# Performance work log

Measured on AMD Instinct MI355X. Metric: run time of the kernel, lower is better.

Reference implementation:

```python
import jax, jax.numpy as jnp
import numpy as np

LOC_SIZE, LOC_EMB = 100000, 256
TIM_SIZE, TIM_EMB = 48, 64
UID_SIZE, UID_EMB = 5000, 128
HID = 512
B, T = 64, 128
L_HIST, G = 1024, 4  # 256 history groups of size 4


def setup_inputs() -> dict:
    key = jax.random.key(0)
    ks = jax.random.split(key, 16)
    s = 0.02
    inp = {
        "loc": jax.random.randint(ks[0], (B, T), 0, LOC_SIZE),
        "tim": jax.random.randint(ks[1], (B, T), 0, TIM_SIZE),
        "input_lengths": jax.random.randint(ks[2], (B,), 1, T + 1),
        "history_loc": jax.random.randint(ks[3], (B, L_HIST), 0, LOC_SIZE),
        "history_tim": jax.random.randint(ks[4], (B, L_HIST), 0, TIM_SIZE),
        "history_uid": jax.random.randint(ks[5], (B, L_HIST), 0, UID_SIZE),
        "group_size": G,
        "emb_loc": jax.random.normal(ks[6], (LOC_SIZE, LOC_EMB), jnp.float32) * s,
        "emb_tim": jax.random.normal(ks[7], (TIM_SIZE, TIM_EMB), jnp.float32) * s,
        "emb_uid": jax.random.normal(ks[8], (UID_SIZE, UID_EMB), jnp.float32) * s,
        "W_attn": jax.random.normal(ks[9], (HID, LOC_EMB + TIM_EMB + UID_EMB), jnp.float32) * s,
        "b_attn": jnp.zeros((HID,), jnp.float32),
        "W_ih": jax.random.normal(ks[10], (3 * HID, LOC_EMB + TIM_EMB), jnp.float32) * s,
        "b_ih": jnp.zeros((3 * HID,), jnp.float32),
        "W_hh": jax.random.normal(ks[11], (3 * HID, HID), jnp.float32) * s,
        "b_hh": jnp.zeros((3 * HID,), jnp.float32),
        "W_final": jax.random.normal(ks[12], (UID_SIZE, 3 * HID), jnp.float32) * s,
        "b_final": jnp.zeros((UID_SIZE,), jnp.float32),
    }
    return inp


def _gru(x_seq, W_ih, b_ih, W_hh, b_hh):
    # x_seq: [T, B, Din] -> outputs [T, B, H], PyTorch gate order (r, z, n)
    H = W_hh.shape[1]
    gx = jnp.einsum("tbd,gd->tbg", x_seq, W_ih) + b_ih  # [T,B,3H]
    h0 = jnp.zeros((x_seq.shape[1], H), x_seq.dtype)

    def step(h, gx_t):
        gh = h @ W_hh.T + b_hh
        xr, xz, xn = jnp.split(gx_t, 3, axis=-1)
        hr, hz, hn = jnp.split(gh, 3, axis=-1)
        r = jax.nn.sigmoid(xr + hr)
        z = jax.nn.sigmoid(xz + hz)
        n = jnp.tanh(xn + r * hn)
        h_new = (1.0 - z) * n + z * h
        return h_new, h_new

    _, outs = jax.lax.scan(step, h0, gx)
    return outs  # [T,B,H]


def reference(loc, tim, input_lengths, history_loc, history_tim, history_uid,
              group_size, emb_loc, emb_tim, emb_uid, W_attn, b_attn,
              W_ih, b_ih, W_hh, b_hh, W_final, b_final):
    Bn, Tn = loc.shape
    # current-trajectory embeddings -> GRU (dropout is identity in eval)
    x = jnp.concatenate([emb_loc[loc], emb_tim[tim]], axis=-1)  # [B,T,Din]
    outs = _gru(jnp.swapaxes(x, 0, 1), W_ih, b_ih, W_hh, b_hh)  # [T,B,H]
    outs = jnp.swapaxes(outs, 0, 1)                              # [B,T,H]
    last = outs[jnp.arange(Bn), input_lengths - 1]               # [B,H]

    # history pooling: groups of size G; uid emb averaged within group,
    # loc/tim embeddings taken at each group's first element
    Gc = group_size
    n_groups = history_uid.shape[1] // Gc
    uid_h = emb_uid[history_uid].reshape(Bn, n_groups, Gc, -1).mean(axis=2)  # [B,N,Du]
    loc_h = emb_loc[history_loc[:, ::Gc]]                                    # [B,N,Dl]
    tim_h = emb_tim[history_tim[:, ::Gc]]                                    # [B,N,Dt]
    hist = jnp.concatenate([loc_h, tim_h, uid_h], axis=-1)
    hist = jnp.tanh(jnp.einsum("bnd,hd->bnh", hist, W_attn) + b_attn)        # [B,N,H]

    # 'dot' attention: replaces the nested python-loop scoring
    energies = jnp.einsum("bh,bnh->bn", last, hist)
    attn_w = jax.nn.softmax(energies, axis=-1)
    context = jnp.einsum("bn,bnh->bh", attn_w, hist)

    out = jnp.concatenate([last, context, last], axis=-1)  # [B,3H]
    y = out @ W_final.T + b_final                          # [B,U]
    # original assigns y (one row) into score[t] of shape [T,U] -> broadcast over T
    score = jnp.broadcast_to(y[:, None, :], (Bn, Tn, y.shape[-1]))
    return score
```

## Files before the change

kernel.cpp:

```cpp
#include <hip/hip_runtime.h>
#include <hip/hip_bf16.h>


typedef __attribute__((ext_vector_type(8))) short bf16x8;
typedef __attribute__((ext_vector_type(4))) float f32x4;
typedef __attribute__((ext_vector_type(4))) unsigned short u16x4;
typedef __attribute__((ext_vector_type(2))) unsigned long long u64x2;
typedef unsigned long long u64;

__device__ inline unsigned short f2bf(float x) {
  __hip_bfloat16 b = __float2bfloat16(x);
  return __builtin_bit_cast(unsigned short, b);
}
__device__ inline bf16x8 pack8(float4 a, float4 b) {
  bf16x8 w;
  w[0]=(short)f2bf(a.x); w[1]=(short)f2bf(a.y); w[2]=(short)f2bf(a.z); w[3]=(short)f2bf(a.w);
  w[4]=(short)f2bf(b.x); w[5]=(short)f2bf(b.y); w[6]=(short)f2bf(b.z); w[7]=(short)f2bf(b.w);
  return w;
}

__global__ __launch_bounds__(256)
void gemm_gx_f(const int* __restrict__ loc, const int* __restrict__ tim,
               const float* __restrict__ eloc, const float* __restrict__ etim,
               const float* __restrict__ W_ih, const float* __restrict__ b_ih,
               float* __restrict__ gx) {
  constexpr int LDR = 40, K = 320, N = 1536;
  __shared__ short Asl[128 * LDR];
  __shared__ short Bsl[128 * LDR];
  const int tid = threadIdx.x;
  const int lane = tid & 63, wid = tid >> 6;
  const int wr = wid >> 1, wc = wid & 1;
  const int m16 = lane & 15, g4 = lane >> 4;
  const int bm = blockIdx.y * 128, bn = blockIdx.x * 128;
  const int srow = tid >> 1, shalf = tid & 1;
  const int grow = bm + srow;
  const int t_ = grow >> 6, b_ = grow & 63;
  const float* aloc = eloc + (size_t)loc[b_ * 128 + t_] * 256 + (shalf << 4);
  const float* atim = etim + (size_t)tim[b_ * 128 + t_] * 64 + (shalf << 4);
  const float* bbase = W_ih + (size_t)(bn + srow) * K + (shalf << 4);
  float4 a0, a1, a2, a3, w0, w1, w2, w3;
  {
    a0 = ((const float4*)aloc)[0]; a1 = ((const float4*)aloc)[1];
    a2 = ((const float4*)aloc)[2]; a3 = ((const float4*)aloc)[3];
    w0 = ((const float4*)bbase)[0]; w1 = ((const float4*)bbase)[1];
    w2 = ((const float4*)bbase)[2]; w3 = ((const float4*)bbase)[3];
  }
  f32x4 acc[4][4] = {};
  for (int k0 = 0; k0 < K; k0 += 32) {
    short* arow = Asl + srow * LDR + (shalf << 4);
    *(bf16x8*)(arow)     = pack8(a0, a1);
    *(bf16x8*)(arow + 8) = pack8(a2, a3);
    short* brow = Bsl + srow * LDR + (shalf << 4);
    *(bf16x8*)(brow)     = pack8(w0, w1);
    *(bf16x8*)(brow + 8) = pack8(w2, w3);
    __syncthreads();
    if (k0 + 32 < K) {
      const int kn = k0 + 32;
      const float* ap = (kn < 256) ? (aloc + kn) : (atim + (kn - 256));
      a0 = ((const float4*)ap)[0]; a1 = ((const float4*)ap)[1];
      a2 = ((const float4*)ap)[2]; a3 = ((const float4*)ap)[3];
      const float* bp = bbase + kn;
      w0 = ((const float4*)bp)[0]; w1 = ((const float4*)bp)[1];
      w2 = ((const float4*)bp)[2]; w3 = ((const float4*)bp)[3];
    }
    bf16x8 af[4], bfr[4];
#pragma unroll
    for (int i = 0; i < 4; ++i) {
      af[i]  = *(const bf16x8*)(Asl + ((wr << 6) + (i << 4) + m16) * LDR + (g4 << 3));
      bfr[i] = *(const bf16x8*)(Bsl + ((wc << 6) + (i << 4) + m16) * LDR + (g4 << 3));
    }
#pragma unroll
    for (int i = 0; i < 4; ++i)
#pragma unroll
      for (int j = 0; j < 4; ++j)
        acc[i][j] = __builtin_amdgcn_mfma_f32_16x16x32_bf16(af[i], bfr[j], acc[i][j], 0, 0, 0);
    __syncthreads();
  }
#pragma unroll
  for (int i = 0; i < 4; ++i)
#pragma unroll
    for (int j = 0; j < 4; ++j) {
      const int col = bn + (wc << 6) + (j << 4) + m16;
      const float bv = b_ih[col];
#pragma unroll
      for (int q = 0; q < 4; ++q) {
        const int row = bm + (wr << 6) + (i << 4) + (g4 << 2) + q;
        gx[(size_t)row * N + col] = acc[i][j][q] + bv;
      }
    }
}

__global__ __launch_bounds__(256)
void gru_attn(const float* __restrict__ gx, const float* __restrict__ W_hh,
              const float* __restrict__ b_hh, const int* __restrict__ lens,
              short* __restrict__ h_bf, float* __restrict__ lastb,
              unsigned int* __restrict__ flags,
              const int* __restrict__ hloc, const int* __restrict__ htim,
              const int* __restrict__ huid,
              const float* __restrict__ eloc, const float* __restrict__ etim,
              const float* __restrict__ euid,
              const float* __restrict__ W_attn, const float* __restrict__ b_attn,
              const float* __restrict__ Wf, float* __restrict__ Wfold,
              float* __restrict__ histt, float* __restrict__ ctx) {
  __shared__ short smem[6 * 16 * 512];
  const int bid = blockIdx.x;
  const int tid = threadIdx.x;

  if (bid < 64) {
    const int grp0 = bid & 3;
    const int b00 = grp0 << 4;
    int tmax = 0;
    for (int i = 0; i < 16; ++i) tmax = max(tmax, lens[b00 + i]);

    if (tid >= 128) {
      for (int t = 0; t < tmax + 1; ++t) __syncthreads();
      return;
    }
    const int lane = tid & 63, tt = tid >> 6;
    const int c = bid >> 2, grp = grp0;
    const int j0 = (c << 5) + (tt << 4);
    const int b0 = b00;
    const int m16 = lane & 15, g4 = lane >> 4;

    for (int gi = 0; gi < 3; ++gi) {
      const float* wg = W_hh + (size_t)(gi * 512 + j0) * 512;
      short* slab = smem + (((gi << 1) + tt) << 13);
      for (int r = 0; r < 16; ++r) {
        int k = lane << 3;
        const float4* src = (const float4*)(wg + (size_t)r * 512 + k);
        int off = ((r << 9) + k) ^ ((r & 7) << 3);
        *(bf16x8*)(slab + off) = pack8(src[0], src[1]);
      }
    }
    __syncthreads();

    const int bcol = b0 + m16;
    const int jr = j0 + (g4 << 2);
    const f32x4 bhr = *(const f32x4*)&b_hh[jr];
    const f32x4 bhz = *(const f32x4*)&b_hh[512 + jr];
    const f32x4 bhn = *(const f32x4*)&b_hh[1024 + jr];
    const int lenb = lens[bcol];
    f32x4 hprev = {0.f, 0.f, 0.f, 0.f};

    unsigned int* gflags = flags + (grp << 8);
    unsigned int* ownflag = gflags + (c << 4);
    unsigned int* bdone = flags + 1024;

    for (int t = 0; t < tmax; ++t) {
      const float* gxb = gx + ((size_t)t * 64 + bcol) * 1536;
      f32x4 gr = *(const f32x4*)(gxb + jr);
      f32x4 gz = *(const f32x4*)(gxb + 512 + jr);
      f32x4 gn = *(const f32x4*)(gxb + 1024 + jr);
      f32x4 ar = {0.f, 0.f, 0.f, 0.f}, az = ar, an = ar;
      if (t) {
        unsigned tgt = (unsigned)t;
        while (true) {
          unsigned f = tgt;
          if (lane < 16)
            f = __hip_atomic_load(gflags + (lane << 4), __ATOMIC_RELAXED, __HIP_MEMORY_SCOPE_AGENT);
          if (__all((int)(f >= tgt))) break;
        }
        asm volatile("" ::: "memory");

        const u64* hp = (const u64*)(h_bf + ((t & 1) << 15) + (size_t)bcol * 512 + (g4 << 3));
        u64 hu[32];
#pragma unroll
        for (int ks = 0; ks < 16; ++ks) {
          hu[2 * ks]     = __hip_atomic_load(hp + ks * 8,     __ATOMIC_RELAXED, __HIP_MEMORY_SCOPE_AGENT);
          hu[2 * ks + 1] = __hip_atomic_load(hp + ks * 8 + 1, __ATOMIC_RELAXED, __HIP_MEMORY_SCOPE_AGENT);
        }
#define GRU_MFMA(ks)                                                                 \
        {                                                                            \
          u64x2 p; p[0] = hu[2 * (ks)]; p[1] = hu[2 * (ks) + 1];                     \
          bf16x8 hf = __builtin_bit_cast(bf16x8, p);                                 \
          int off = ((m16 << 9) + ((ks) << 5) + (g4 << 3)) ^ ((m16 & 7) << 3);       \
          ar = __builtin_amdgcn_mfma_f32_16x16x32_bf16(*(const bf16x8*)(smem + ((0 + tt) << 13) + off), hf, ar, 0, 0, 0); \
          az = __builtin_amdgcn_mfma_f32_16x16x32_bf16(*(const bf16x8*)(smem + ((2 + tt) << 13) + off), hf, az, 0, 0, 0); \
          an = __builtin_amdgcn_mfma_f32_16x16x32_bf16(*(const bf16x8*)(smem + ((4 + tt) << 13) + off), hf, an, 0, 0, 0); \
        }
        GRU_MFMA(0)  GRU_MFMA(1)  GRU_MFMA(2)  GRU_MFMA(3)
        GRU_MFMA(4)  GRU_MFMA(5)  GRU_MFMA(6)  GRU_MFMA(7)
        GRU_MFMA(8)  GRU_MFMA(9)  GRU_MFMA(10) GRU_MFMA(11)
        GRU_MFMA(12) GRU_MFMA(13) GRU_MFMA(14) GRU_MFMA(15)
#undef GRU_MFMA
      }
      u16x4 hw;
#pragma unroll
      for (int q = 0; q < 4; ++q) {
        float r = 1.f / (1.f + __expf(-(gr[q] + ar[q] + bhr[q])));
        float z = 1.f / (1.f + __expf(-(gz[q] + az[q] + bhz[q])));
        float xn = gn[q] + r * (an[q] + bhn[q]);
        float n = 1.f - 2.f / (__expf(2.f * xn) + 1.f);
        float hv = (1.f - z) * n + z * hprev[q];
        hprev[q] = hv;
        hw[q] = f2bf(hv);
      }
      __hip_atomic_store((u64*)(h_bf + ((~t & 1) << 15) + (size_t)bcol * 512 + jr),
                         __builtin_bit_cast(u64, hw),
                         __ATOMIC_RELAXED, __HIP_MEMORY_SCOPE_AGENT);
      if (t == lenb - 1) {
        *(f32x4*)(lastb + (size_t)bcol * 512 + jr) = hprev;
      }
      if (t < tmax - 1) {
        asm volatile("s_waitcnt vmcnt(0)" ::: "memory");
        __syncthreads();
        if (tid == 0) {
          __hip_atomic_store(ownflag, (unsigned)(t + 1), __ATOMIC_RELAXED, __HIP_MEMORY_SCOPE_AGENT);
          for (int i = 0; i < 16; ++i)
            if (lens[b0 + i] == t + 1)
              __hip_atomic_fetch_add(bdone + ((b0 + i) << 4), 1u,
                                     __ATOMIC_RELAXED, __HIP_MEMORY_SCOPE_AGENT);
        }
      }
    }
    asm volatile("s_waitcnt vmcnt(0)" ::: "memory");
    __syncthreads();
    if (tid == 0) {
      for (int i = 0; i < 16; ++i)
        if (lens[b0 + i] == tmax)
          __hip_atomic_fetch_add(bdone + ((b0 + i) << 4), 1u,
                                 __ATOMIC_RELAXED, __HIP_MEMORY_SCOPE_AGENT);
    }
    return;
  }

  {
    constexpr int LDR = 40, K = 448, N = 512;
    short* Asl = smem;
    short* Bsl = smem + 128 * LDR;
    const int lane = tid & 63, wid = tid >> 6;
    const int wr = wid >> 1, wc = wid & 1;
    const int m16 = lane & 15, g4 = lane >> 4;
    const int srow = tid >> 1, shalf = tid & 1;
    for (int tile = bid - 64; tile < 512; tile += 128) {
      const int yt = tile >> 2, nt = tile & 3;
      const int bm = yt << 7, bn = nt << 7;
      f32x4 acc[4][4] = {};
      for (int k0 = 0; k0 < K; k0 += 32) {
        {
          const int grow = bm + srow;
          const int b = grow >> 8, n = grow & 255;
          const int base = b * 1024 + (n << 2);
          float4 f0, f1, f2, f3;
          if (k0 < 256) {
            const float* ap = eloc + (size_t)hloc[base] * 256 + k0 + (shalf << 4);
            f0 = ((const float4*)ap)[0]; f1 = ((const float4*)ap)[1];
            f2 = ((const float4*)ap)[2]; f3 = ((const float4*)ap)[3];
          } else if (k0 < 320) {
            const float* ap = etim + (size_t)htim[base] * 64 + (k0 - 256) + (shalf << 4);
            f0 = ((const float4*)ap)[0]; f1 = ((const float4*)ap)[1];
            f2 = ((const float4*)ap)[2]; f3 = ((const float4*)ap)[3];
          } else {
            const int cu = (k0 - 320) + (shalf << 4);
            const float4* u0 = (const float4*)(euid + (size_t)huid[base + 0] * 128 + cu);
            const float4* u1 = (const float4*)(euid + (size_t)huid[base + 1] * 128 + cu);
            const float4* u2 = (const float4*)(euid + (size_t)huid[base + 2] * 128 + cu);
            const float4* u3 = (const float4*)(euid + (size_t)huid[base + 3] * 128 + cu);
#define AVG4(idx, dst) { float4 a=u0[idx],b4=u1[idx],c4=u2[idx],d4=u3[idx];            \
            dst.x=0.25f*(a.x+b4.x+c4.x+d4.x); dst.y=0.25f*(a.y+b4.y+c4.y+d4.y);       \
            dst.z=0.25f*(a.z+b4.z+c4.z+d4.z); dst.w=0.25f*(a.w+b4.w+c4.w+d4.w); }
            AVG4(0, f0) AVG4(1, f1) AVG4(2, f2) AVG4(3, f3)
#undef AVG4
          }
          short* arow = Asl + srow * LDR + (shalf << 4);
          *(bf16x8*)(arow)     = pack8(f0, f1);
          *(bf16x8*)(arow + 8) = pack8(f2, f3);
          const float* bp = W_attn + (size_t)(bn + srow) * K + k0 + (shalf << 4);
          f0 = ((const float4*)bp)[0]; f1 = ((const float4*)bp)[1];
          f2 = ((const float4*)bp)[2]; f3 = ((const float4*)bp)[3];
          short* brow = Bsl + srow * LDR + (shalf << 4);
          *(bf16x8*)(brow)     = pack8(f0, f1);
          *(bf16x8*)(brow + 8) = pack8(f2, f3);
        }
        __syncthreads();
        bf16x8 af[4], bfr[4];
#pragma unroll
        for (int i = 0; i < 4; ++i) {
          af[i]  = *(const bf16x8*)(Asl + ((wr << 6) + (i << 4) + m16) * LDR + (g4 << 3));
          bfr[i] = *(const bf16x8*)(Bsl + ((wc << 6) + (i << 4) + m16) * LDR + (g4 << 3));
        }
#pragma unroll
        for (int i = 0; i < 4; ++i)
#pragma unroll
          for (int j = 0; j < 4; ++j)
            acc[i][j] = __builtin_amdgcn_mfma_f32_16x16x32_bf16(af[i], bfr[j], acc[i][j], 0, 0, 0);
        __syncthreads();
      }
#pragma unroll
      for (int i = 0; i < 4; ++i)
#pragma unroll
        for (int j = 0; j < 4; ++j) {
          const int col = bn + (wc << 6) + (j << 4) + m16;
          const float bv = b_attn[col];
#pragma unroll
          for (int q = 0; q < 4; ++q) {
            const int row = bm + (wr << 6) + (i << 4) + (g4 << 2) + q;
            histt[(size_t)row * N + col] = tanhf(acc[i][j][q] + bv);
          }
        }
    }
    asm volatile("s_waitcnt vmcnt(0)" ::: "memory");
    if (tid == 0)
      __hip_atomic_fetch_add(flags + 2048, 1u, __ATOMIC_RELEASE, __HIP_MEMORY_SCOPE_AGENT);

    for (int u = bid - 64; u < 5000; u += 128) {
      const int cc = tid << 1;
      float2 a = *(const float2*)(Wf + (size_t)u * 1536 + cc);
      float2 b2 = *(const float2*)(Wf + (size_t)u * 1536 + 1024 + cc);
      float2 o; o.x = a.x + b2.x; o.y = a.y + b2.y;
      *(float2*)(Wfold + (size_t)u * 512 + cc) = o;
    }
  }

  if (bid < 128) {
    const int b = bid - 64;
    if (tid == 0) {
      while (__hip_atomic_load(flags + 2048, __ATOMIC_RELAXED, __HIP_MEMORY_SCOPE_AGENT) < 128u)
        __builtin_amdgcn_s_sleep(7);
      while (__hip_atomic_load(flags + 1024 + (b << 4), __ATOMIC_RELAXED, __HIP_MEMORY_SCOPE_AGENT) < 16u)
        __builtin_amdgcn_s_sleep(7);
    }
    __syncthreads();
    __builtin_amdgcn_fence(__ATOMIC_ACQUIRE, "agent");
    float* ls  = (float*)smem;
    float* wv  = ls + 512;
    float* red = wv + 256;
    ((float2*)ls)[tid] = ((const float2*)(lastb + (size_t)b * 512))[tid];
    __syncthreads();
    const float* hb = histt + (size_t)b * 256 * 512;
    const float* hrow = hb + (size_t)tid * 512;
    float acc = 0.f;
    for (int k = 0; k < 512; k += 4) {
      float4 h4 = *(const float4*)(hrow + k);
      acc += ls[k] * h4.x + ls[k + 1] * h4.y + ls[k + 2] * h4.z + ls[k + 3] * h4.w;
    }
    red[tid] = acc;
    __syncthreads();
    for (int s = 128; s; s >>= 1) {
      if (tid < s) red[tid] = fmaxf(red[tid], red[tid + s]);
      __syncthreads();
    }
    float m = red[0];
    __syncthreads();
    float ex = expf(acc - m);
    wv[tid] = ex; red[tid] = ex;
    __syncthreads();
    for (int s = 128; s; s >>= 1) {
      if (tid < s) red[tid] += red[tid + s];
      __syncthreads();
    }
    float inv = 1.f / red[0];
    float c0 = 0.f, c1 = 0.f;
    for (int n = 0; n < 256; ++n) {
      float wn = wv[n];
      c0 += wn * hb[(size_t)n * 512 + tid];
      c1 += wn * hb[(size_t)n * 512 + tid + 256];
    }
    ctx[(size_t)b * 512 + tid]       = c0 * inv;
    ctx[(size_t)b * 512 + tid + 256] = c1 * inv;
  }
}

__global__ __launch_bounds__(256)
void final_gemm(const float* __restrict__ last, const float* __restrict__ ctx,
                const float* __restrict__ Wfold, const float* __restrict__ Wf,
                const float* __restrict__ bf, float* __restrict__ y) {
  __shared__ float s[64][132];
  const int tid = threadIdx.x;
  const int u0 = blockIdx.x << 3;
  const int ul = tid >> 6, b = tid & 63;
  float acc0 = 0.f, acc1 = 0.f;
  for (int kc = 0; kc < 8; ++kc) {
    __syncthreads();
    for (int i = tid; i < 2048; i += 256) {
      int rb = i >> 5, cc = (i & 31) << 2;
      int k = kc * 128 + cc;
      const float* src = (k < 512) ? (last + (size_t)rb * 512 + k)
                                   : (ctx + (size_t)rb * 512 + k - 512);
      *(float4*)&s[rb][cc] = *(const float4*)src;
    }
    __syncthreads();
#pragma unroll
    for (int uu = 0; uu < 2; ++uu) {
      int u = u0 + ul + uu * 4;
      const float* wrow = (kc < 4) ? (Wfold + (size_t)u * 512 + kc * 128)
                                   : (Wf + (size_t)u * 1536 + 512 + (kc - 4) * 128);
      float a = 0.f;
#pragma unroll 8
      for (int c = 0; c < 128; c += 4) {
        float4 w4 = *(const float4*)(wrow + c);
        float4 s4 = *(const float4*)&s[b][c];
        a += w4.x * s4.x + w4.y * s4.y + w4.z * s4.z + w4.w * s4.w;
      }
      if (uu == 0) acc0 += a; else acc1 += a;
    }
  }
  int u = u0 + ul;
  y[(size_t)b * 5000 + u]     = acc0 + bf[u];
  y[(size_t)b * 5000 + u + 4] = acc1 + bf[u + 4];
}

__global__ void broadcast_y(const float* __restrict__ y, float* __restrict__ out) {
  int bt = blockIdx.x;
  const float4* src = (const float4*)(y + (size_t)(bt >> 7) * 5000);
  float4* dst = (float4*)(out + (size_t)bt * 5000);
  for (int i = threadIdx.x; i < 1250; i += 256) dst[i] = src[i];
}

extern "C" void kernel_launch(void* const* d_in, const int* in_sizes, int n_in,
                              void* d_out, int out_size, void* d_ws, size_t ws_size,
                              hipStream_t stream) {
  const int* loc  = (const int*)d_in[0];
  const int* tim  = (const int*)d_in[1];
  const int* lens = (const int*)d_in[2];
  const int* hloc = (const int*)d_in[3];
  const int* htim = (const int*)d_in[4];
  const int* huid = (const int*)d_in[5];
  const float* eloc    = (const float*)d_in[7];
  const float* etim    = (const float*)d_in[8];
  const float* euid    = (const float*)d_in[9];
  const float* W_attn  = (const float*)d_in[10];
  const float* b_attn  = (const float*)d_in[11];
  const float* W_ih    = (const float*)d_in[12];
  const float* b_ih    = (const float*)d_in[13];
  const float* W_hh    = (const float*)d_in[14];
  const float* b_hh    = (const float*)d_in[15];
  const float* W_final = (const float*)d_in[16];
  const float* b_final = (const float*)d_in[17];
  float* out = (float*)d_out;
  char* ws = (char*)d_ws;

  float* gx    = (float*)(ws + 0ull);
  float* histt = (float*)(ws + 50331648ull);
  float* lastb = (float*)(ws + 83886080ull);
  float* ctx   = (float*)(ws + 84017152ull);
  float* yv    = (float*)(ws + 84148224ull);
  short* h_bf  = (short*)(ws + 85428224ull);
  unsigned int* flags = (unsigned int*)(ws + 85559296ull);
  float* Wfold = (float*)(ws + 85571584ull);

  hipMemsetAsync(flags, 0, 12288, stream);
  gemm_gx_f<<<dim3(12, 64), 256, 0, stream>>>(loc, tim, eloc, etim, W_ih, b_ih, gx);

  gru_attn<<<192, 256, 0, stream>>>(gx, W_hh, b_hh, lens, h_bf, lastb, flags,
                                    hloc, htim, huid, eloc, etim, euid,
                                    W_attn, b_attn, W_final, Wfold, histt, ctx);

  final_gemm<<<625, 256, 0, stream>>>(lastb, ctx, Wfold, W_final, b_final, yv);
  broadcast_y<<<8192, 256, 0, stream>>>(yv, out);
}
```

Measured before the change: 594.1 us.

## Fuse input-gate GEMM into persistent GRU kernel with per-timestep readiness flags

```diff
diff --git a/kernel.cpp b/kernel.cpp
--- a/kernel.cpp
+++ b/kernel.cpp
@@ -20,88 +20,19 @@
 }
 
 __global__ __launch_bounds__(256)
-void gemm_gx_f(const int* __restrict__ loc, const int* __restrict__ tim,
-               const float* __restrict__ eloc, const float* __restrict__ etim,
-               const float* __restrict__ W_ih, const float* __restrict__ b_ih,
-               float* __restrict__ gx) {
-  constexpr int LDR = 40, K = 320, N = 1536;
-  __shared__ short Asl[128 * LDR];
-  __shared__ short Bsl[128 * LDR];
-  const int tid = threadIdx.x;
-  const int lane = tid & 63, wid = tid >> 6;
-  const int wr = wid >> 1, wc = wid & 1;
-  const int m16 = lane & 15, g4 = lane >> 4;
-  const int bm = blockIdx.y * 128, bn = blockIdx.x * 128;
-  const int srow = tid >> 1, shalf = tid & 1;
-  const int grow = bm + srow;
-  const int t_ = grow >> 6, b_ = grow & 63;
-  const float* aloc = eloc + (size_t)loc[b_ * 128 + t_] * 256 + (shalf << 4);
-  const float* atim = etim + (size_t)tim[b_ * 128 + t_] * 64 + (shalf << 4);
-  const float* bbase = W_ih + (size_t)(bn + srow) * K + (shalf << 4);
-  float4 a0, a1, a2, a3, w0, w1, w2, w3;
-  {
-    a0 = ((const float4*)aloc)[0]; a1 = ((const float4*)aloc)[1];
-    a2 = ((const float4*)aloc)[2]; a3 = ((const float4*)aloc)[3];
-    w0 = ((const float4*)bbase)[0]; w1 = ((const float4*)bbase)[1];
-    w2 = ((const float4*)bbase)[2]; w3 = ((const float4*)bbase)[3];
-  }
-  f32x4 acc[4][4] = {};
-  for (int k0 = 0; k0 < K; k0 += 32) {
-    short* arow = Asl + srow * LDR + (shalf << 4);
-    *(bf16x8*)(arow)     = pack8(a0, a1);
-    *(bf16x8*)(arow + 8) = pack8(a2, a3);
-    short* brow = Bsl + srow * LDR + (shalf << 4);
-    *(bf16x8*)(brow)     = pack8(w0, w1);
-    *(bf16x8*)(brow + 8) = pack8(w2, w3);
-    __syncthreads();
-    if (k0 + 32 < K) {
-      const int kn = k0 + 32;
-      const float* ap = (kn < 256) ? (aloc + kn) : (atim + (kn - 256));
-      a0 = ((const float4*)ap)[0]; a1 = ((const float4*)ap)[1];
-      a2 = ((const float4*)ap)[2]; a3 = ((const float4*)ap)[3];
-      const float* bp = bbase + kn;
-      w0 = ((const float4*)bp)[0]; w1 = ((const float4*)bp)[1];
-      w2 = ((const float4*)bp)[2]; w3 = ((const float4*)bp)[3];
-    }
-    bf16x8 af[4], bfr[4];
-#pragma unroll
-    for (int i = 0; i < 4; ++i) {
-      af[i]  = *(const bf16x8*)(Asl + ((wr << 6) + (i << 4) + m16) * LDR + (g4 << 3));
-      bfr[i] = *(const bf16x8*)(Bsl + ((wc << 6) + (i << 4) + m16) * LDR + (g4 << 3));
-    }
-#pragma unroll
-    for (int i = 0; i < 4; ++i)
-#pragma unroll
-      for (int j = 0; j < 4; ++j)
-        acc[i][j] = __builtin_amdgcn_mfma_f32_16x16x32_bf16(af[i], bfr[j], acc[i][j], 0, 0, 0);
-    __syncthreads();
-  }
-#pragma unroll
-  for (int i = 0; i < 4; ++i)
-#pragma unroll
-    for (int j = 0; j < 4; ++j) {
-      const int col = bn + (wc << 6) + (j << 4) + m16;
-      const float bv = b_ih[col];
-#pragma unroll
-      for (int q = 0; q < 4; ++q) {
-        const int row = bm + (wr << 6) + (i << 4) + (g4 << 2) + q;
-        gx[(size_t)row * N + col] = acc[i][j][q] + bv;
-      }
-    }
-}
-
-__global__ __launch_bounds__(256)
-void gru_attn(const float* __restrict__ gx, const float* __restrict__ W_hh,
+void gru_attn(const float* __restrict__ W_hh,
               const float* __restrict__ b_hh, const int* __restrict__ lens,
               short* __restrict__ h_bf, float* __restrict__ lastb,
               unsigned int* __restrict__ flags,
+              const int* __restrict__ loc, const int* __restrict__ tim,
               const int* __restrict__ hloc, const int* __restrict__ htim,
               const int* __restrict__ huid,
               const float* __restrict__ eloc, const float* __restrict__ etim,
               const float* __restrict__ euid,
+              const float* __restrict__ W_ih, const float* __restrict__ b_ih,
               const float* __restrict__ W_attn, const float* __restrict__ b_attn,
               const float* __restrict__ Wf, float* __restrict__ Wfold,
-              float* __restrict__ histt, float* __restrict__ ctx) {
+              float* __restrict__ gx, float* __restrict__ histt, float* __restrict__ ctx) {
   __shared__ short smem[6 * 16 * 512];
   const int bid = blockIdx.x;
   const int tid = threadIdx.x;
@@ -145,12 +76,31 @@
     unsigned int* gflags = flags + (grp << 8);
     unsigned int* ownflag = gflags + (c << 4);
     unsigned int* bdone = flags + 1024;
+    unsigned int* gxdone = flags + 2048;
 
     for (int t = 0; t < tmax; ++t) {
-      const float* gxb = gx + ((size_t)t * 64 + bcol) * 1536;
-      f32x4 gr = *(const f32x4*)(gxb + jr);
-      f32x4 gz = *(const f32x4*)(gxb + 512 + jr);
-      f32x4 gn = *(const f32x4*)(gxb + 1024 + jr);
+      if (!(t & 1)) {
+        if (lane == 0) {
+          while (__hip_atomic_load(gxdone + ((t >> 1) << 4), __ATOMIC_RELAXED,
+                                   __HIP_MEMORY_SCOPE_AGENT) < 12u)
+            __builtin_amdgcn_s_sleep(1);
+        }
+        asm volatile("" ::: "memory");
+      }
+      const u64* gxp = (const u64*)(gx + ((size_t)t * 64 + bcol) * 1536 + jr);
+      u64 g0 = __hip_atomic_load(gxp,       __ATOMIC_RELAXED, __HIP_MEMORY_SCOPE_AGENT);
+      u64 g1 = __hip_atomic_load(gxp + 1,   __ATOMIC_RELAXED, __HIP_MEMORY_SCOPE_AGENT);
+      u64 g2 = __hip_atomic_load(gxp + 256, __ATOMIC_RELAXED, __HIP_MEMORY_SCOPE_AGENT);
+      u64 g3 = __hip_atomic_load(gxp + 257, __ATOMIC_RELAXED, __HIP_MEMORY_SCOPE_AGENT);
+      u64 g4v= __hip_atomic_load(gxp + 512, __ATOMIC_RELAXED, __HIP_MEMORY_SCOPE_AGENT);
+      u64 g5 = __hip_atomic_load(gxp + 513, __ATOMIC_RELAXED, __HIP_MEMORY_SCOPE_AGENT);
+      u64x2 p0; p0[0] = g0; p0[1] = g1;
+      u64x2 p1; p1[0] = g2; p1[1] = g3;
+      u64x2 p2; p2[0] = g4v; p2[1] = g5;
+      f32x4 gr = __builtin_bit_cast(f32x4, p0);
+      f32x4 gz = __builtin_bit_cast(f32x4, p1);
+      f32x4 gn = __builtin_bit_cast(f32x4, p2);
+
       f32x4 ar = {0.f, 0.f, 0.f, 0.f}, az = ar, an = ar;
       if (t) {
         unsigned tgt = (unsigned)t;
@@ -218,8 +168,83 @@
     if (tid == 0) {
       for (int i = 0; i < 16; ++i)
         if (lens[b0 + i] == tmax)
-          __hip_atomic_fetch_add(bdone + ((b0 + i) << 4), 1u,
+          __hip_atomic_fetch_add(flags + 1024 + ((b0 + i) << 4), 1u,
                                  __ATOMIC_RELAXED, __HIP_MEMORY_SCOPE_AGENT);
+    }
+    return;
+  }
+
+  if (bid < 192) {
+    constexpr int LDR = 40, K = 320, N = 1536;
+    short* Asl = smem;
+    short* Bsl = smem + 128 * LDR;
+    const int lane = tid & 63, wid = tid >> 6;
+    const int wr = wid >> 1, wc = wid & 1;
+    const int m16 = lane & 15, g4 = lane >> 4;
+    const int srow = tid >> 1, shalf = tid & 1;
+    for (int tile = bid - 64; tile < 768; tile += 128) {
+      const int yt = tile / 12, nt = tile % 12;
+      const int bm = yt << 7, bn = nt << 7;
+      const int grow = bm + srow;
+      const int t_ = grow >> 6, b_ = grow & 63;
+      const float* aloc = eloc + (size_t)loc[b_ * 128 + t_] * 256 + (shalf << 4);
+      const float* atim = etim + (size_t)tim[b_ * 128 + t_] * 64 + (shalf << 4);
+      const float* bbase = W_ih + (size_t)(bn + srow) * K + (shalf << 4);
+      float4 a0 = ((const float4*)aloc)[0], a1 = ((const float4*)aloc)[1];
+      float4 a2 = ((const float4*)aloc)[2], a3 = ((const float4*)aloc)[3];
+      float4 w0 = ((const float4*)bbase)[0], w1 = ((const float4*)bbase)[1];
+      float4 w2 = ((const float4*)bbase)[2], w3 = ((const float4*)bbase)[3];
+      f32x4 acc[4][4] = {};
+      for (int k0 = 0; k0 < K; k0 += 32) {
+        short* arow = Asl + srow * LDR + (shalf << 4);
+        *(bf16x8*)(arow)     = pack8(a0, a1);
+        *(bf16x8*)(arow + 8) = pack8(a2, a3);
+        short* brow = Bsl + srow * LDR + (shalf << 4);
+        *(bf16x8*)(brow)     = pack8(w0, w1);
+        *(bf16x8*)(brow + 8) = pack8(w2, w3);
+        __syncthreads();
+        if (k0 + 32 < K) {
+          const int kn = k0 + 32;
+          const float* ap = (kn < 256) ? (aloc + kn) : (atim + (kn - 256));
+          a0 = ((const float4*)ap)[0]; a1 = ((const float4*)ap)[1];
+          a2 = ((const float4*)ap)[2]; a3 = ((const float4*)ap)[3];
+          const float* bp = bbase + kn;
+          w0 = ((const float4*)bp)[0]; w1 = ((const float4*)bp)[1];
+          w2 = ((const float4*)bp)[2]; w3 = ((const float4*)bp)[3];
+        }
+        bf16x8 af[4], bfr[4];
+#pragma unroll
+        for (int i = 0; i < 4; ++i) {
+          af[i]  = *(const bf16x8*)(Asl + ((wr << 6) + (i << 4) + m16) * LDR + (g4 << 3));
+          bfr[i] = *(const bf16x8*)(Bsl + ((wc << 6) + (i << 4) + m16) * LDR + (g4 << 3));
+        }
+#pragma unroll
+        for (int i = 0; i < 4; ++i)
+#pragma unroll
+          for (int j = 0; j < 4; ++j)
+            acc[i][j] = __builtin_amdgcn_mfma_f32_16x16x32_bf16(af[i], bfr[j], acc[i][j], 0, 0, 0);
+        __syncthreads();
+      }
+#pragma unroll
+      for (int i = 0; i < 4; ++i)
+#pragma unroll
+        for (int j = 0; j < 4; ++j) {
+          const int col = bn + (wc << 6) + (j << 4) + m16;
+          const float bv = b_ih[col];
+#pragma unroll
+          for (int q = 0; q < 4; ++q) {
+            const int row = bm + (wr << 6) + (i << 4) + (g4 << 2) + q;
+            float v = acc[i][j][q] + bv;
+            __hip_atomic_store((unsigned*)(gx + (size_t)row * N + col),
+                               __builtin_bit_cast(unsigned, v),
+                               __ATOMIC_RELAXED, __HIP_MEMORY_SCOPE_AGENT);
+          }
+        }
+      asm volatile("s_waitcnt vmcnt(0)" ::: "memory");
+      __syncthreads();
+      if (tid == 0)
+        __hip_atomic_fetch_add(flags + 2048 + (yt << 4), 1u,
+                               __ATOMIC_RELAXED, __HIP_MEMORY_SCOPE_AGENT);
     }
     return;
   }
@@ -232,7 +257,7 @@
     const int wr = wid >> 1, wc = wid & 1;
     const int m16 = lane & 15, g4 = lane >> 4;
     const int srow = tid >> 1, shalf = tid & 1;
-    for (int tile = bid - 64; tile < 512; tile += 128) {
+    for (int tile = bid - 192; tile < 512; tile += 64) {
       const int yt = tile >> 2, nt = tile & 3;
       const int bm = yt << 7, bn = nt << 7;
       f32x4 acc[4][4] = {};
@@ -301,9 +326,9 @@
     }
     asm volatile("s_waitcnt vmcnt(0)" ::: "memory");
     if (tid == 0)
-      __hip_atomic_fetch_add(flags + 2048, 1u, __ATOMIC_RELEASE, __HIP_MEMORY_SCOPE_AGENT);
-
-    for (int u = bid - 64; u < 5000; u += 128) {
+      __hip_atomic_fetch_add(flags + 3072, 1u, __ATOMIC_RELEASE, __HIP_MEMORY_SCOPE_AGENT);
+
+    for (int u = bid - 192; u < 5000; u += 64) {
       const int cc = tid << 1;
       float2 a = *(const float2*)(Wf + (size_t)u * 1536 + cc);
       float2 b2 = *(const float2*)(Wf + (size_t)u * 1536 + 1024 + cc);
@@ -312,10 +337,10 @@
     }
   }
 
-  if (bid < 128) {
-    const int b = bid - 64;
+  {
+    const int b = bid - 192;
     if (tid == 0) {
-      while (__hip_atomic_load(flags + 2048, __ATOMIC_RELAXED, __HIP_MEMORY_SCOPE_AGENT) < 128u)
+      while (__hip_atomic_load(flags + 3072, __ATOMIC_RELAXED, __HIP_MEMORY_SCOPE_AGENT) < 64u)
         __builtin_amdgcn_s_sleep(7);
       while (__hip_atomic_load(flags + 1024 + (b << 4), __ATOMIC_RELAXED, __HIP_MEMORY_SCOPE_AGENT) < 16u)
         __builtin_amdgcn_s_sleep(7);
@@ -437,14 +462,13 @@
   float* yv    = (float*)(ws + 84148224ull);
   short* h_bf  = (short*)(ws + 85428224ull);
   unsigned int* flags = (unsigned int*)(ws + 85559296ull);
-  float* Wfold = (float*)(ws + 85571584ull);
-
-  hipMemsetAsync(flags, 0, 12288, stream);
-  gemm_gx_f<<<dim3(12, 64), 256, 0, stream>>>(loc, tim, eloc, etim, W_ih, b_ih, gx);
-
-  gru_attn<<<192, 256, 0, stream>>>(gx, W_hh, b_hh, lens, h_bf, lastb, flags,
-                                    hloc, htim, huid, eloc, etim, euid,
-                                    W_attn, b_attn, W_final, Wfold, histt, ctx);
+  float* Wfold = (float*)(ws + 85575680ull);
+
+  hipMemsetAsync(flags, 0, 16384, stream);
+  gru_attn<<<256, 256, 0, stream>>>(W_hh, b_hh, lens, h_bf, lastb, flags,
+                                    loc, tim, hloc, htim, huid, eloc, etim, euid,
+                                    W_ih, b_ih, W_attn, b_attn, W_final, Wfold,
+                                    gx, histt, ctx);
 
   final_gemm<<<625, 256, 0, stream>>>(lastb, ctx, Wfold, W_final, b_final, yv);
   broadcast_y<<<8192, 256, 0, stream>>>(yv, out);
```

Result: no change. 604.6 us (+1.8%).
